# Kernel optimization log

Hardware: AMD Instinct MI355X
Metric: run time of the kernel (lower is better)

The kernel has to match this reference:

```python
import jax, jax.numpy as jnp
import numpy as np

MARGIN = 1.0

def setup_inputs() -> dict:
    key = jax.random.key(0)
    k1, k2 = jax.random.split(key)
    B, D, NUM_CLASSES = 4096, 512, 64
    inputs = jax.random.normal(k1, (B, D), dtype=jnp.float32)
    labels = jax.random.randint(k2, (B,), 0, NUM_CLASSES, dtype=jnp.int64)
    return {"inputs": inputs, "labels": labels}

def reference(inputs, labels):
    # Full pairwise squared L2 distances via the ||a-b||^2 = ||a||^2 + ||b||^2 - 2 a.b expansion
    sq = jnp.sum(inputs * inputs, axis=1)                      # [B]
    d2 = sq[:, None] + sq[None, :] - 2.0 * (inputs @ inputs.T)  # [B, B]
    d2 = jnp.maximum(d2, 0.0)
    # Safe sqrt: zero (self) distances get exactly 0 without NaN-producing sqrt(0) grads
    nz = d2 > 1e-12
    dist = jnp.where(nz, jnp.sqrt(jnp.where(nz, d2, 1.0)), 0.0)  # [B, B]

    mask = labels[:, None] == labels[None, :]                   # [B, B] same-class mask (includes self)
    mask_f = mask.astype(dist.dtype)

    # Per-anchor: mean distance to positives (self included, contributing 0, as in the torch loop)
    ap_mean = jnp.sum(dist * mask_f, axis=1) / jnp.sum(mask_f, axis=1)  # [B]
    # Per-anchor: min distance to negatives
    an_min = jnp.min(jnp.where(mask, jnp.inf, dist), axis=1)            # [B]

    tmp = ap_mean - an_min + MARGIN                             # [B]
    # `if tmp > 0: loss += tmp` over the batch == sum of relu(tmp)
    return jnp.sum(jnp.maximum(tmp, 0.0))
```

## Files before the change

kernel.cpp:

```cpp
#include <hip/hip_runtime.h>
#include <hip/hip_bf16.h>

typedef unsigned char u8;
typedef unsigned short u16;
typedef unsigned int u32;
typedef unsigned long long u64;
typedef __attribute__((ext_vector_type(4))) float f32x4;

#define B_SZ 4096
#define D_SZ 512
#define NCLS 64
#define BK   64
#define NKK  (D_SZ / BK)
#define NT   32
#define NBLK (NT * (NT + 1) / 2)
#define TILE_BYTES (128 * BK)

#define WAITV4()  asm volatile("s_waitcnt vmcnt(4)" ::: "memory")
#define WAITV0()  asm volatile("s_waitcnt vmcnt(0)" ::: "memory")
#define BARRIER() asm volatile("s_barrier" ::: "memory")


__device__ __forceinline__ u8 f2fp8(float x) {
    union { float f; u32 u; } a; a.f = x;
    u32 s = (a.u >> 24) & 0x80u;
    u32 m = a.u & 0x7fffffffu;
    u32 r = m + 0x7ffffu + ((m >> 20) & 1u);
    int e = (int)(r >> 23) - 127 + 7;
    u32 mant = (r >> 20) & 7u;
    if (e <= 0) return (u8)s;
    if (e >= 16) return (u8)(s | 0x7Eu);
    return (u8)(s | ((u32)e << 3) | mant);
}

__device__ __forceinline__ void gload16(const void* g, void* l) {
    __builtin_amdgcn_global_load_lds(
        (const __attribute__((address_space(1))) u32*)g,
        (__attribute__((address_space(3))) u32*)l,
        16, 0, 0);
}

__device__ __forceinline__ void stage_fp8(const u8* __restrict__ gsrc, u8* dst, int t) {
    #pragma unroll
    for (int q = 0; q < 2; ++q) {
        const int s = t + q * 256;
        const int r = s >> 2;
        const int c16 = (s & 3) ^ (r & 3);
        gload16(gsrc + (size_t)r * D_SZ + (c16 << 4), dst + s * 16);
    }
}


__global__ __launch_bounds__(256) void prep_kernel(
    const float* __restrict__ in, u8* __restrict__ bf8,
    float* __restrict__ sq, float* __restrict__ ap_sum, u32* __restrict__ an_min)
{
    const int wave = threadIdx.x >> 6, l = threadIdx.x & 63;
    const int row = blockIdx.x * 4 + wave;
    const float* p = in + (size_t)row * D_SZ + l * 8;
    float4 v0 = *(const float4*)p;
    float4 v1 = *(const float4*)(p + 4);
    float s = v0.x*v0.x + v0.y*v0.y + v0.z*v0.z + v0.w*v0.w
            + v1.x*v1.x + v1.y*v1.y + v1.z*v1.z + v1.w*v1.w;
    u64 pk =  (u64)f2fp8(v0.x)
           | ((u64)f2fp8(v0.y) << 8)
           | ((u64)f2fp8(v0.z) << 16)
           | ((u64)f2fp8(v0.w) << 24)
           | ((u64)f2fp8(v1.x) << 32)
           | ((u64)f2fp8(v1.y) << 40)
           | ((u64)f2fp8(v1.z) << 48)
           | ((u64)f2fp8(v1.w) << 56);
    *(u64*)(bf8 + (size_t)row * D_SZ + l * 8) = pk;
    #pragma unroll
    for (int off = 1; off < 64; off <<= 1) s += __shfl_xor(s, off);
    if (l == 0) {
        sq[row] = s;
        ap_sum[row] = 0.0f;
        an_min[row] = 0x7f800000u;
    }
}


__global__ __launch_bounds__(256) void tile_kernel(
    const u8* __restrict__ bf8, const int* __restrict__ lab,
    const float* __restrict__ sq, float* __restrict__ ap_sum, u32* __restrict__ an_min)
{
    __shared__ u8 As[3][TILE_BYTES];
    __shared__ u8 Bs[3][TILE_BYTES];
    __shared__ float sqA[128], sqB[128];
    __shared__ int labA[128], labB[128];

    const int t = threadIdx.x;

    int bid = blockIdx.x;
    bid = (bid & 7) * (NBLK / 8) + (bid >> 3);

    int tm = (int)((__builtin_sqrtf(8.0f * (float)bid + 1.0f) - 1.0f) * 0.5f);
    while ((tm + 1) * (tm + 2) / 2 <= bid) ++tm;
    while (tm * (tm + 1) / 2 > bid) --tm;
    const int tn = bid - tm * (tm + 1) / 2;
    const bool diag = (tm == tn);

    const int rowBase = tm * 128;
    const int colBase = tn * 128;

    if (t < 128) { labA[t] = lab[rowBase + t]; sqA[t] = sq[rowBase + t]; }
    else { int u = t - 128; labB[u] = lab[colBase + u]; sqB[u] = sq[colBase + u]; }

    const int wave = t >> 6, lane = t & 63;
    const int wr = wave >> 1, wc = wave & 1;
    const int g = lane >> 4, c = lane & 15;

    f32x4 acc[4][4];
    #pragma unroll
    for (int i = 0; i < 4; ++i)
        #pragma unroll
        for (int j = 0; j < 4; ++j)
            acc[i][j] = (f32x4){0.f, 0.f, 0.f, 0.f};

    const u8* gA = bf8 + (size_t)rowBase * D_SZ;
    const u8* gB = bf8 + (size_t)colBase * D_SZ;

    __syncthreads();

    stage_fp8(gA,      As[0], t);
    stage_fp8(gB,      Bs[0], t);
    stage_fp8(gA + BK, As[1], t);
    stage_fp8(gB + BK, Bs[1], t);

    const int x3 = c & 3, sub = (g & 1) * 8, gh = g >> 1;

    #pragma unroll
    for (int kk = 0; kk < NKK; ++kk) {
        if (kk < NKK - 1) { WAITV4(); }
        else              { WAITV0(); }
        BARRIER();

        if (kk + 2 < NKK) {
            stage_fp8(gA + (kk + 2) * BK, As[(kk + 2) % 3], t);
            stage_fp8(gB + (kk + 2) * BK, Bs[(kk + 2) % 3], t);
        }

        const u8* abuf = As[kk % 3];
        const u8* bbuf = Bs[kk % 3];

        #pragma unroll
        for (int ks = 0; ks < 2; ++ks) {
            const int koff = (((ks * 2 + gh) ^ x3) << 4) + sub;
            long a[4], b[4];
            #pragma unroll
            for (int mi = 0; mi < 4; ++mi)
                a[mi] = *(const long*)(abuf + (wr * 64 + mi * 16 + c) * BK + koff);
            #pragma unroll
            for (int ni = 0; ni < 4; ++ni)
                b[ni] = *(const long*)(bbuf + (wc * 64 + ni * 16 + c) * BK + koff);
            #pragma unroll
            for (int mi = 0; mi < 4; ++mi)
                #pragma unroll
                for (int ni = 0; ni < 4; ++ni)
                    acc[mi][ni] = __builtin_amdgcn_mfma_f32_16x16x32_fp8_fp8(a[mi], b[ni], acc[mi][ni], 0, 0, 0);
        }
    }

    float sc[4], mc[4];
    #pragma unroll
    for (int ni = 0; ni < 4; ++ni) { sc[ni] = 0.0f; mc[ni] = __builtin_inff(); }

    #pragma unroll
    for (int mi = 0; mi < 4; ++mi) {
        #pragma unroll
        for (int r = 0; r < 4; ++r) {
            const int lrow = wr * 64 + mi * 16 + g * 4 + r;
            const int i = rowBase + lrow;
            const int li = labA[lrow];
            const float sqi = sqA[lrow];
            float s = 0.0f;
            float mn = __builtin_inff();
            #pragma unroll
            for (int ni = 0; ni < 4; ++ni) {
                const int lcol = wc * 64 + ni * 16 + c;
                float d2 = sqi + sqB[lcol] - 2.0f * acc[mi][ni][r];
                d2 = fmaxf(d2, 0.0f);
                float dist = (d2 > 1e-12f) ? __builtin_sqrtf(d2) : 0.0f;
                if (diag && lrow == lcol) dist = 0.0f;
                if (li == labB[lcol]) { s += dist; sc[ni] += dist; }
                else                  { mn = fminf(mn, dist); mc[ni] = fminf(mc[ni], dist); }
            }
            #pragma unroll
            for (int off = 1; off < 16; off <<= 1) {
                s += __shfl_xor(s, off);
                mn = fminf(mn, __shfl_xor(mn, off));
            }
            if (c == 0) {
                atomicAdd(&ap_sum[i], s);
                atomicMin(&an_min[i], __float_as_uint(mn));
            }
        }
    }

    if (!diag) {
        #pragma unroll
        for (int ni = 0; ni < 4; ++ni) {
            float s = sc[ni], mn = mc[ni];
            s += __shfl_xor(s, 16); s += __shfl_xor(s, 32);
            mn = fminf(mn, __shfl_xor(mn, 16)); mn = fminf(mn, __shfl_xor(mn, 32));
            if (lane < 16) {
                const int j = colBase + wc * 64 + ni * 16 + c;
                atomicAdd(&ap_sum[j], s);
                atomicMin(&an_min[j], __float_as_uint(mn));
            }
        }
    }
}


__global__ __launch_bounds__(1024) void final_kernel(
    const float* __restrict__ ap_sum, const u32* __restrict__ an_min,
    const int* __restrict__ lab, float* __restrict__ out)
{
    __shared__ int cnt[NCLS];
    __shared__ float wsum[16];
    const int t = threadIdx.x;
    if (t < NCLS) cnt[t] = 0;
    __syncthreads();
    for (int i = t; i < B_SZ; i += 1024) atomicAdd(&cnt[lab[i]], 1);
    __syncthreads();
    float v = 0.0f;
    for (int i = t; i < B_SZ; i += 1024) {
        float apm = ap_sum[i] / (float)cnt[lab[i]];
        float anm = __uint_as_float(an_min[i]);
        v += fmaxf(apm - anm + 1.0f, 0.0f);
    }
    #pragma unroll
    for (int off = 1; off < 64; off <<= 1) v += __shfl_xor(v, off);
    if ((t & 63) == 0) wsum[t >> 6] = v;
    __syncthreads();
    if (t == 0) {
        float s = 0.0f;
        #pragma unroll
        for (int w = 0; w < 16; ++w) s += wsum[w];
        out[0] = s;
    }
}


extern "C" void kernel_launch(void* const* d_in, const int* in_sizes, int n_in,
                              void* d_out, int out_size, void* d_ws, size_t ws_size,
                              hipStream_t stream) {
    const float* inputs = (const float*)d_in[0];
    const int* labels = (const int*)d_in[1];
    float* out = (float*)d_out;

    char* ws = (char*)d_ws;
    float* ap_sum = (float*)ws;
    u32* an_min = (u32*)(ws + 16384);
    float* sq = (float*)(ws + 32768);
    u8* bf8 = (u8*)(ws + 65536);

    prep_kernel<<<dim3(B_SZ / 4), dim3(256), 0, stream>>>(inputs, bf8, sq, ap_sum, an_min);
    tile_kernel<<<dim3(NBLK), dim3(256), 0, stream>>>(bf8, labels, sq, ap_sum, an_min);
    final_kernel<<<dim3(1), dim3(1024), 0, stream>>>(ap_sum, an_min, labels, out);
}
```

Baseline: 39.53 us.

## Compute full square tile grid instead of symmetric triangle, simplify pipeline

```diff
diff --git a/kernel.cpp b/kernel.cpp
--- a/kernel.cpp
+++ b/kernel.cpp
@@ -2,7 +2,6 @@
 #include <hip/hip_bf16.h>
 
 typedef unsigned char u8;
-typedef unsigned short u16;
 typedef unsigned int u32;
 typedef unsigned long long u64;
 typedef __attribute__((ext_vector_type(4))) float f32x4;
@@ -13,12 +12,8 @@
 #define BK   64
 #define NKK  (D_SZ / BK)
 #define NT   32
-#define NBLK (NT * (NT + 1) / 2)
+#define NBLK (NT * NT)
 #define TILE_BYTES (128 * BK)
-
-#define WAITV4()  asm volatile("s_waitcnt vmcnt(4)" ::: "memory")
-#define WAITV0()  asm volatile("s_waitcnt vmcnt(0)" ::: "memory")
-#define BARRIER() asm volatile("s_barrier" ::: "memory")
 
 
 __device__ __forceinline__ u8 f2fp8(float x) {
@@ -85,22 +80,14 @@
     const u8* __restrict__ bf8, const int* __restrict__ lab,
     const float* __restrict__ sq, float* __restrict__ ap_sum, u32* __restrict__ an_min)
 {
-    __shared__ u8 As[3][TILE_BYTES];
-    __shared__ u8 Bs[3][TILE_BYTES];
+    __shared__ u8 As[2][TILE_BYTES];
+    __shared__ u8 Bs[2][TILE_BYTES];
     __shared__ float sqA[128], sqB[128];
     __shared__ int labA[128], labB[128];
 
     const int t = threadIdx.x;
-
-    int bid = blockIdx.x;
-    bid = (bid & 7) * (NBLK / 8) + (bid >> 3);
-
-    int tm = (int)((__builtin_sqrtf(8.0f * (float)bid + 1.0f) - 1.0f) * 0.5f);
-    while ((tm + 1) * (tm + 2) / 2 <= bid) ++tm;
-    while (tm * (tm + 1) / 2 > bid) --tm;
-    const int tn = bid - tm * (tm + 1) / 2;
-    const bool diag = (tm == tn);
-
+    const int tm = blockIdx.x & 31;
+    const int tn = blockIdx.x >> 5;
     const int rowBase = tm * 128;
     const int colBase = tn * 128;
 
@@ -121,28 +108,22 @@
     const u8* gA = bf8 + (size_t)rowBase * D_SZ;
     const u8* gB = bf8 + (size_t)colBase * D_SZ;
 
-    __syncthreads();
-
-    stage_fp8(gA,      As[0], t);
-    stage_fp8(gB,      Bs[0], t);
-    stage_fp8(gA + BK, As[1], t);
-    stage_fp8(gB + BK, Bs[1], t);
+    stage_fp8(gA, As[0], t);
+    stage_fp8(gB, Bs[0], t);
 
     const int x3 = c & 3, sub = (g & 1) * 8, gh = g >> 1;
 
-    #pragma unroll
+    #pragma unroll 1
     for (int kk = 0; kk < NKK; ++kk) {
-        if (kk < NKK - 1) { WAITV4(); }
-        else              { WAITV0(); }
-        BARRIER();
-
-        if (kk + 2 < NKK) {
-            stage_fp8(gA + (kk + 2) * BK, As[(kk + 2) % 3], t);
-            stage_fp8(gB + (kk + 2) * BK, Bs[(kk + 2) % 3], t);
+        __syncthreads();
+
+        if (kk + 1 < NKK) {
+            stage_fp8(gA + (kk + 1) * BK, As[(kk + 1) & 1], t);
+            stage_fp8(gB + (kk + 1) * BK, Bs[(kk + 1) & 1], t);
         }
 
-        const u8* abuf = As[kk % 3];
-        const u8* bbuf = Bs[kk % 3];
+        const u8* abuf = As[kk & 1];
+        const u8* bbuf = Bs[kk & 1];
 
         #pragma unroll
         for (int ks = 0; ks < 2; ++ks) {
@@ -161,10 +142,6 @@
                     acc[mi][ni] = __builtin_amdgcn_mfma_f32_16x16x32_fp8_fp8(a[mi], b[ni], acc[mi][ni], 0, 0, 0);
         }
     }
-
-    float sc[4], mc[4];
-    #pragma unroll
-    for (int ni = 0; ni < 4; ++ni) { sc[ni] = 0.0f; mc[ni] = __builtin_inff(); }
 
     #pragma unroll
     for (int mi = 0; mi < 4; ++mi) {
@@ -179,12 +156,13 @@
             #pragma unroll
             for (int ni = 0; ni < 4; ++ni) {
                 const int lcol = wc * 64 + ni * 16 + c;
+                const int j = colBase + lcol;
                 float d2 = sqi + sqB[lcol] - 2.0f * acc[mi][ni][r];
                 d2 = fmaxf(d2, 0.0f);
                 float dist = (d2 > 1e-12f) ? __builtin_sqrtf(d2) : 0.0f;
-                if (diag && lrow == lcol) dist = 0.0f;
-                if (li == labB[lcol]) { s += dist; sc[ni] += dist; }
-                else                  { mn = fminf(mn, dist); mc[ni] = fminf(mc[ni], dist); }
+                if (i == j) dist = 0.0f;
+                if (li == labB[lcol]) s += dist;
+                else                  mn = fminf(mn, dist);
             }
             #pragma unroll
             for (int off = 1; off < 16; off <<= 1) {
@@ -194,20 +172,6 @@
             if (c == 0) {
                 atomicAdd(&ap_sum[i], s);
                 atomicMin(&an_min[i], __float_as_uint(mn));
-            }
-        }
-    }
-
-    if (!diag) {
-        #pragma unroll
-        for (int ni = 0; ni < 4; ++ni) {
-            float s = sc[ni], mn = mc[ni];
-            s += __shfl_xor(s, 16); s += __shfl_xor(s, 32);
-            mn = fminf(mn, __shfl_xor(mn, 16)); mn = fminf(mn, __shfl_xor(mn, 32));
-            if (lane < 16) {
-                const int j = colBase + wc * 64 + ni * 16 + c;
-                atomicAdd(&ap_sum[j], s);
-                atomicMin(&an_min[j], __float_as_uint(mn));
             }
         }
     }
```

Result: slower. 49.54 us (+25.3%).

## Prefetch all K slices into LDS upfront instead of triple-buffered pipeline

Applied to the files above, without the earlier changes.

```diff
diff --git a/kernel.cpp b/kernel.cpp
--- a/kernel.cpp
+++ b/kernel.cpp
@@ -2,7 +2,6 @@
 #include <hip/hip_bf16.h>
 
 typedef unsigned char u8;
-typedef unsigned short u16;
 typedef unsigned int u32;
 typedef unsigned long long u64;
 typedef __attribute__((ext_vector_type(4))) float f32x4;
@@ -16,8 +15,7 @@
 #define NBLK (NT * (NT + 1) / 2)
 #define TILE_BYTES (128 * BK)
 
-#define WAITV4()  asm volatile("s_waitcnt vmcnt(4)" ::: "memory")
-#define WAITV0()  asm volatile("s_waitcnt vmcnt(0)" ::: "memory")
+#define WAITN(n)  asm volatile("s_waitcnt vmcnt(" #n ")" ::: "memory")
 #define BARRIER() asm volatile("s_barrier" ::: "memory")
 
 
@@ -81,14 +79,18 @@
 }
 
 
+extern __shared__ char smem[];
+
 __global__ __launch_bounds__(256) void tile_kernel(
     const u8* __restrict__ bf8, const int* __restrict__ lab,
     const float* __restrict__ sq, float* __restrict__ ap_sum, u32* __restrict__ an_min)
 {
-    __shared__ u8 As[3][TILE_BYTES];
-    __shared__ u8 Bs[3][TILE_BYTES];
-    __shared__ float sqA[128], sqB[128];
-    __shared__ int labA[128], labB[128];
+    u8* As = (u8*)smem;
+    u8* Bs = As + NKK * TILE_BYTES;
+    float* sqA = (float*)(smem + 131072);
+    float* sqB = sqA + 128;
+    int* labA  = (int*)(smem + 132096);
+    int* labB  = labA + 128;
 
     const int t = threadIdx.x;
 
@@ -123,26 +125,28 @@
 
     __syncthreads();
 
-    stage_fp8(gA,      As[0], t);
-    stage_fp8(gB,      Bs[0], t);
-    stage_fp8(gA + BK, As[1], t);
-    stage_fp8(gB + BK, Bs[1], t);
+    #pragma unroll
+    for (int k = 0; k < NKK; ++k) {
+        stage_fp8(gA + k * BK, As + k * TILE_BYTES, t);
+        stage_fp8(gB + k * BK, Bs + k * TILE_BYTES, t);
+    }
 
     const int x3 = c & 3, sub = (g & 1) * 8, gh = g >> 1;
 
     #pragma unroll
     for (int kk = 0; kk < NKK; ++kk) {
-        if (kk < NKK - 1) { WAITV4(); }
-        else              { WAITV0(); }
+        if      (kk == 0) WAITN(28);
+        else if (kk == 1) WAITN(24);
+        else if (kk == 2) WAITN(20);
+        else if (kk == 3) WAITN(16);
+        else if (kk == 4) WAITN(12);
+        else if (kk == 5) WAITN(8);
+        else if (kk == 6) WAITN(4);
+        else              WAITN(0);
         BARRIER();
 
-        if (kk + 2 < NKK) {
-            stage_fp8(gA + (kk + 2) * BK, As[(kk + 2) % 3], t);
-            stage_fp8(gB + (kk + 2) * BK, Bs[(kk + 2) % 3], t);
-        }
-
-        const u8* abuf = As[kk % 3];
-        const u8* bbuf = Bs[kk % 3];
+        const u8* abuf = As + kk * TILE_BYTES;
+        const u8* bbuf = Bs + kk * TILE_BYTES;
 
         #pragma unroll
         for (int ks = 0; ks < 2; ++ks) {
@@ -257,7 +261,9 @@
     float* sq = (float*)(ws + 32768);
     u8* bf8 = (u8*)(ws + 65536);
 
+    const int smem_bytes = NKK * TILE_BYTES * 2 + 2048;
+
     prep_kernel<<<dim3(B_SZ / 4), dim3(256), 0, stream>>>(inputs, bf8, sq, ap_sum, an_min);
-    tile_kernel<<<dim3(NBLK), dim3(256), 0, stream>>>(bf8, labels, sq, ap_sum, an_min);
+    tile_kernel<<<dim3(NBLK), dim3(256), smem_bytes, stream>>>(bf8, labels, sq, ap_sum, an_min);
     final_kernel<<<dim3(1), dim3(1024), 0, stream>>>(ap_sum, an_min, labels, out);
 }
```

Measured after the change: 61.89 us. +56.6%, slower.
